# Kernel optimization log

Measured on AMD Instinct MI355X. Metric: run time of the kernel, lower is better.

The kernel has to match this reference:

```python
import jax, jax.numpy as jnp
import numpy as np
from jax import lax

B, C_IN, H, W = 8, 32, 48, 48
C_OUT = 32
K = 3
DEPTH = C_IN * K * K          # 288
L = H * W                      # 2304 (stride=1, pad=1, dil=1 -> same spatial size)


def setup_inputs() -> dict:
    key = jax.random.key(0)
    k1, k2, k3 = jax.random.split(key, 3)
    x = jax.random.normal(k1, (B, C_IN, H, W), dtype=jnp.float32)
    # per-spatial-location unshared weights, same layout as the torch module
    weight = jax.random.normal(k2, (1, DEPTH, L, C_OUT), dtype=jnp.float32) * 0.05
    bias = jax.random.normal(k3, (1, C_OUT, H, W), dtype=jnp.float32) * 0.05
    return {"x": x, "weight": weight, "bias": bias}


def reference(x, weight, bias):
    # unfold: (B, C*K*K, H_out, W_out), channel-major (C, kh, kw) order matches torch unfold
    patches = lax.conv_general_dilated_patches(
        x,
        filter_shape=(K, K),
        window_strides=(1, 1),
        padding=((1, 1), (1, 1)),
        rhs_dilation=(1, 1),
    )
    patches = patches.reshape(B, DEPTH, L)  # (B, depth, L)
    w = weight[0]  # (depth, L, out)
    # fused per-location matmul instead of torch's broadcast-mul + sum
    out = jnp.einsum("bdl,dlo->bol", patches, w)  # (B, out, L)
    return out.reshape(B, C_OUT, H, W) + bias
```

## Files before the change

### kernel.cpp

```cpp
#include <hip/hip_runtime.h>


constexpr int NB    = 8;
constexpr int CIN   = 32;
constexpr int HWD   = 48;
constexpr int COUT  = 32;
constexpr int DEPTH = 288;
constexpr int LTOT  = 2304;
constexpr int LB    = 4;
constexpr int NBLK  = LTOT / LB;
constexpr int PL    = DEPTH * NB + 8;
constexpr int WSTR  = LTOT * COUT;

__global__ __launch_bounds__(256, 3) void lc2d(const float* __restrict__ x,
                                               const float* __restrict__ wgt,
                                               const float* __restrict__ bias,
                                               float* __restrict__ out) {
    __shared__ float patches[LB * PL];
    __shared__ float red[4 * NB * LB * COUT];

    const int tid = threadIdx.x;
    const int bid   = blockIdx.x;
    const int ltile = (bid & 7) * (NBLK / 8) + (bid >> 3);
    const int l0    = ltile * LB;
    const int h0    = l0 / HWD;
    const int w0    = l0 - h0 * HWD;

    #pragma unroll
    for (int k = 0; k < (LB * DEPTH * NB) / 256; ++k) {
        const int sidx = k * 256 + tid;
        const int b  = sidx & 7;
        const int t2 = sidx >> 3;
        const int d  = t2 % DEPTH;
        const int ls = t2 / DEPTH;
        const int c  = d / 9;
        const int r9 = d - c * 9;
        const int kh = r9 / 3;
        const int kw = r9 - kh * 3;
        const int ih = h0 + kh - 1;
        const int iw = w0 + ls + kw - 1;
        float v = 0.f;
        if ((unsigned)ih < (unsigned)HWD && (unsigned)iw < (unsigned)HWD)
            v = x[((b * CIN + c) * HWD + ih) * HWD + iw];
        patches[ls * PL + d * NB + b] = v;
    }
    __syncthreads();

    const int wave = tid >> 6;
    const int lane = tid & 63;
    const int og   = lane & 7;
    const int lsub = (lane >> 3) & 3;
    const int dpar = lane >> 5;
    const int d0   = wave * 72 + dpar * 36;

    const float* wp    = wgt + (size_t)d0 * WSTR + (size_t)(l0 + lsub) * COUT + og * 4;
    const float* pbase = &patches[lsub * PL + d0 * NB];

    float4 acc[NB];
    #pragma unroll
    for (int b = 0; b < NB; ++b) acc[b] = make_float4(0.f, 0.f, 0.f, 0.f);

    float4 wc[4], wn[4];
    #pragma unroll
    for (int j = 0; j < 4; ++j)
        wc[j] = *reinterpret_cast<const float4*>(wp + (size_t)j * WSTR);

    for (int ch = 0; ch < 8; ++ch) {
        #pragma unroll
        for (int j = 0; j < 4; ++j)
            wn[j] = *reinterpret_cast<const float4*>(wp + (size_t)((ch + 1) * 4 + j) * WSTR);
        #pragma unroll
        for (int j = 0; j < 4; ++j) {
            const int i = ch * 4 + j;
            const float4 p0 = *reinterpret_cast<const float4*>(pbase + i * NB);
            const float4 p1 = *reinterpret_cast<const float4*>(pbase + i * NB + 4);
            acc[0].x = fmaf(p0.x, wc[j].x, acc[0].x); acc[0].y = fmaf(p0.x, wc[j].y, acc[0].y);
            acc[0].z = fmaf(p0.x, wc[j].z, acc[0].z); acc[0].w = fmaf(p0.x, wc[j].w, acc[0].w);
            acc[1].x = fmaf(p0.y, wc[j].x, acc[1].x); acc[1].y = fmaf(p0.y, wc[j].y, acc[1].y);
            acc[1].z = fmaf(p0.y, wc[j].z, acc[1].z); acc[1].w = fmaf(p0.y, wc[j].w, acc[1].w);
            acc[2].x = fmaf(p0.z, wc[j].x, acc[2].x); acc[2].y = fmaf(p0.z, wc[j].y, acc[2].y);
            acc[2].z = fmaf(p0.z, wc[j].z, acc[2].z); acc[2].w = fmaf(p0.z, wc[j].w, acc[2].w);
            acc[3].x = fmaf(p0.w, wc[j].x, acc[3].x); acc[3].y = fmaf(p0.w, wc[j].y, acc[3].y);
            acc[3].z = fmaf(p0.w, wc[j].z, acc[3].z); acc[3].w = fmaf(p0.w, wc[j].w, acc[3].w);
            acc[4].x = fmaf(p1.x, wc[j].x, acc[4].x); acc[4].y = fmaf(p1.x, wc[j].y, acc[4].y);
            acc[4].z = fmaf(p1.x, wc[j].z, acc[4].z); acc[4].w = fmaf(p1.x, wc[j].w, acc[4].w);
            acc[5].x = fmaf(p1.y, wc[j].x, acc[5].x); acc[5].y = fmaf(p1.y, wc[j].y, acc[5].y);
            acc[5].z = fmaf(p1.y, wc[j].z, acc[5].z); acc[5].w = fmaf(p1.y, wc[j].w, acc[5].w);
            acc[6].x = fmaf(p1.z, wc[j].x, acc[6].x); acc[6].y = fmaf(p1.z, wc[j].y, acc[6].y);
            acc[6].z = fmaf(p1.z, wc[j].z, acc[6].z); acc[6].w = fmaf(p1.z, wc[j].w, acc[6].w);
            acc[7].x = fmaf(p1.w, wc[j].x, acc[7].x); acc[7].y = fmaf(p1.w, wc[j].y, acc[7].y);
            acc[7].z = fmaf(p1.w, wc[j].z, acc[7].z); acc[7].w = fmaf(p1.w, wc[j].w, acc[7].w);
        }
        #pragma unroll
        for (int j = 0; j < 4; ++j) wc[j] = wn[j];
    }
    #pragma unroll
    for (int j = 0; j < 4; ++j) {
        const int i = 32 + j;
        const float4 p0 = *reinterpret_cast<const float4*>(pbase + i * NB);
        const float4 p1 = *reinterpret_cast<const float4*>(pbase + i * NB + 4);
        acc[0].x = fmaf(p0.x, wc[j].x, acc[0].x); acc[0].y = fmaf(p0.x, wc[j].y, acc[0].y);
        acc[0].z = fmaf(p0.x, wc[j].z, acc[0].z); acc[0].w = fmaf(p0.x, wc[j].w, acc[0].w);
        acc[1].x = fmaf(p0.y, wc[j].x, acc[1].x); acc[1].y = fmaf(p0.y, wc[j].y, acc[1].y);
        acc[1].z = fmaf(p0.y, wc[j].z, acc[1].z); acc[1].w = fmaf(p0.y, wc[j].w, acc[1].w);
        acc[2].x = fmaf(p0.z, wc[j].x, acc[2].x); acc[2].y = fmaf(p0.z, wc[j].y, acc[2].y);
        acc[2].z = fmaf(p0.z, wc[j].z, acc[2].z); acc[2].w = fmaf(p0.z, wc[j].w, acc[2].w);
        acc[3].x = fmaf(p0.w, wc[j].x, acc[3].x); acc[3].y = fmaf(p0.w, wc[j].y, acc[3].y);
        acc[3].z = fmaf(p0.w, wc[j].z, acc[3].z); acc[3].w = fmaf(p0.w, wc[j].w, acc[3].w);
        acc[4].x = fmaf(p1.x, wc[j].x, acc[4].x); acc[4].y = fmaf(p1.x, wc[j].y, acc[4].y);
        acc[4].z = fmaf(p1.x, wc[j].z, acc[4].z); acc[4].w = fmaf(p1.x, wc[j].w, acc[4].w);
        acc[5].x = fmaf(p1.y, wc[j].x, acc[5].x); acc[5].y = fmaf(p1.y, wc[j].y, acc[5].y);
        acc[5].z = fmaf(p1.y, wc[j].z, acc[5].z); acc[5].w = fmaf(p1.y, wc[j].w, acc[5].w);
        acc[6].x = fmaf(p1.z, wc[j].x, acc[6].x); acc[6].y = fmaf(p1.z, wc[j].y, acc[6].y);
        acc[6].z = fmaf(p1.z, wc[j].z, acc[6].z); acc[6].w = fmaf(p1.z, wc[j].w, acc[6].w);
        acc[7].x = fmaf(p1.w, wc[j].x, acc[7].x); acc[7].y = fmaf(p1.w, wc[j].y, acc[7].y);
        acc[7].z = fmaf(p1.w, wc[j].z, acc[7].z); acc[7].w = fmaf(p1.w, wc[j].w, acc[7].w);
    }

    #pragma unroll
    for (int b = 0; b < NB; ++b) {
        acc[b].x += __shfl_xor(acc[b].x, 32);
        acc[b].y += __shfl_xor(acc[b].y, 32);
        acc[b].z += __shfl_xor(acc[b].z, 32);
        acc[b].w += __shfl_xor(acc[b].w, 32);
    }
    if (lane < 32) {
        #pragma unroll
        for (int b = 0; b < NB; ++b)
            *reinterpret_cast<float4*>(&red[(((wave * NB) + b) * LB + lsub) * COUT + og * 4]) = acc[b];
    }
    __syncthreads();

    const int ob = tid >> 5;
    const int oo = tid & 31;
    float s[LB];
    #pragma unroll
    for (int l = 0; l < LB; ++l)
        s[l] = red[((0 * NB + ob) * LB + l) * COUT + oo]
             + red[((1 * NB + ob) * LB + l) * COUT + oo]
             + red[((2 * NB + ob) * LB + l) * COUT + oo]
             + red[((3 * NB + ob) * LB + l) * COUT + oo];
    const float4 bv = *reinterpret_cast<const float4*>(bias + (size_t)oo * LTOT + l0);
    const float4 o4 = make_float4(s[0] + bv.x, s[1] + bv.y, s[2] + bv.z, s[3] + bv.w);
    *reinterpret_cast<float4*>(out + ((size_t)(ob * COUT + oo)) * LTOT + l0) = o4;
}

extern "C" void kernel_launch(void* const* d_in, const int* in_sizes, int n_in,
                              void* d_out, int out_size, void* d_ws, size_t ws_size,
                              hipStream_t stream) {
    const float* x    = (const float*)d_in[0];
    const float* wgt  = (const float*)d_in[1];
    const float* bias = (const float*)d_in[2];
    float* out        = (float*)d_out;
    lc2d<<<NBLK, 256, 0, stream>>>(x, wgt, bias, out);
}
```

Baseline: 29.90 us.

## Alias reduction buffer onto patch LDS and deepen weight prefetch to three stages

The reduction scratch now reuses the patches shared-memory buffer, with an extra barrier before it is overwritten. This cuts LDS per block so four blocks fit per CU instead of three, and the launch bounds are raised to match. The weight loads move from double-buffered to triple-buffered register prefetch, keeping more global loads in flight. The deeper prefetch and higher occupancy target both push on register pressure, which could lead to spills.

```diff
diff --git a/kernel.cpp b/kernel.cpp
--- a/kernel.cpp
+++ b/kernel.cpp
@@ -12,12 +12,42 @@
 constexpr int PL    = DEPTH * NB + 8;
 constexpr int WSTR  = LTOT * COUT;
 
-__global__ __launch_bounds__(256, 3) void lc2d(const float* __restrict__ x,
+#define FMAS(P0, P1, WV)                                                        \
+    acc[0].x = fmaf((P0).x, (WV).x, acc[0].x); acc[0].y = fmaf((P0).x, (WV).y, acc[0].y); \
+    acc[0].z = fmaf((P0).x, (WV).z, acc[0].z); acc[0].w = fmaf((P0).x, (WV).w, acc[0].w); \
+    acc[1].x = fmaf((P0).y, (WV).x, acc[1].x); acc[1].y = fmaf((P0).y, (WV).y, acc[1].y); \
+    acc[1].z = fmaf((P0).y, (WV).z, acc[1].z); acc[1].w = fmaf((P0).y, (WV).w, acc[1].w); \
+    acc[2].x = fmaf((P0).z, (WV).x, acc[2].x); acc[2].y = fmaf((P0).z, (WV).y, acc[2].y); \
+    acc[2].z = fmaf((P0).z, (WV).z, acc[2].z); acc[2].w = fmaf((P0).z, (WV).w, acc[2].w); \
+    acc[3].x = fmaf((P0).w, (WV).x, acc[3].x); acc[3].y = fmaf((P0).w, (WV).y, acc[3].y); \
+    acc[3].z = fmaf((P0).w, (WV).z, acc[3].z); acc[3].w = fmaf((P0).w, (WV).w, acc[3].w); \
+    acc[4].x = fmaf((P1).x, (WV).x, acc[4].x); acc[4].y = fmaf((P1).x, (WV).y, acc[4].y); \
+    acc[4].z = fmaf((P1).x, (WV).z, acc[4].z); acc[4].w = fmaf((P1).x, (WV).w, acc[4].w); \
+    acc[5].x = fmaf((P1).y, (WV).x, acc[5].x); acc[5].y = fmaf((P1).y, (WV).y, acc[5].y); \
+    acc[5].z = fmaf((P1).y, (WV).z, acc[5].z); acc[5].w = fmaf((P1).y, (WV).w, acc[5].w); \
+    acc[6].x = fmaf((P1).z, (WV).x, acc[6].x); acc[6].y = fmaf((P1).z, (WV).y, acc[6].y); \
+    acc[6].z = fmaf((P1).z, (WV).z, acc[6].z); acc[6].w = fmaf((P1).z, (WV).w, acc[6].w); \
+    acc[7].x = fmaf((P1).w, (WV).x, acc[7].x); acc[7].y = fmaf((P1).w, (WV).y, acc[7].y); \
+    acc[7].z = fmaf((P1).w, (WV).z, acc[7].z); acc[7].w = fmaf((P1).w, (WV).w, acc[7].w);
+
+#define PRELOAD(W, CH)                                                          \
+    { _Pragma("unroll") for (int j = 0; j < 4; ++j)                             \
+        W[j] = *reinterpret_cast<const float4*>(wp + (size_t)((CH) * 4 + j) * WSTR); }
+
+#define COMPUTE(W, CH)                                                          \
+    { _Pragma("unroll") for (int j = 0; j < 4; ++j) {                           \
+        const int i = (CH) * 4 + j;                                             \
+        const float4 p0 = *reinterpret_cast<const float4*>(pbase + i * NB);     \
+        const float4 p1 = *reinterpret_cast<const float4*>(pbase + i * NB + 4); \
+        FMAS(p0, p1, W[j]); } }
+
+__global__ __launch_bounds__(256, 4) void lc2d(const float* __restrict__ x,
                                                const float* __restrict__ wgt,
                                                const float* __restrict__ bias,
                                                float* __restrict__ out) {
-    __shared__ float patches[LB * PL];
-    __shared__ float red[4 * NB * LB * COUT];
+    __shared__ float lds[LB * PL];
+    float* const patches = lds;
+    float* const red     = lds;
 
     const int tid = threadIdx.x;
     const int bid   = blockIdx.x;
@@ -60,62 +90,15 @@
     #pragma unroll
     for (int b = 0; b < NB; ++b) acc[b] = make_float4(0.f, 0.f, 0.f, 0.f);
 
-    float4 wc[4], wn[4];
+    float4 wA[4], wB[4], wC[4];
+    PRELOAD(wA, 0) PRELOAD(wB, 1) PRELOAD(wC, 2)
     #pragma unroll
-    for (int j = 0; j < 4; ++j)
-        wc[j] = *reinterpret_cast<const float4*>(wp + (size_t)j * WSTR);
-
-    for (int ch = 0; ch < 8; ++ch) {
-        #pragma unroll
-        for (int j = 0; j < 4; ++j)
-            wn[j] = *reinterpret_cast<const float4*>(wp + (size_t)((ch + 1) * 4 + j) * WSTR);
-        #pragma unroll
-        for (int j = 0; j < 4; ++j) {
-            const int i = ch * 4 + j;
-            const float4 p0 = *reinterpret_cast<const float4*>(pbase + i * NB);
-            const float4 p1 = *reinterpret_cast<const float4*>(pbase + i * NB + 4);
-            acc[0].x = fmaf(p0.x, wc[j].x, acc[0].x); acc[0].y = fmaf(p0.x, wc[j].y, acc[0].y);
-            acc[0].z = fmaf(p0.x, wc[j].z, acc[0].z); acc[0].w = fmaf(p0.x, wc[j].w, acc[0].w);
-            acc[1].x = fmaf(p0.y, wc[j].x, acc[1].x); acc[1].y = fmaf(p0.y, wc[j].y, acc[1].y);
-            acc[1].z = fmaf(p0.y, wc[j].z, acc[1].z); acc[1].w = fmaf(p0.y, wc[j].w, acc[1].w);
-            acc[2].x = fmaf(p0.z, wc[j].x, acc[2].x); acc[2].y = fmaf(p0.z, wc[j].y, acc[2].y);
-            acc[2].z = fmaf(p0.z, wc[j].z, acc[2].z); acc[2].w = fmaf(p0.z, wc[j].w, acc[2].w);
-            acc[3].x = fmaf(p0.w, wc[j].x, acc[3].x); acc[3].y = fmaf(p0.w, wc[j].y, acc[3].y);
-            acc[3].z = fmaf(p0.w, wc[j].z, acc[3].z); acc[3].w = fmaf(p0.w, wc[j].w, acc[3].w);
-            acc[4].x = fmaf(p1.x, wc[j].x, acc[4].x); acc[4].y = fmaf(p1.x, wc[j].y, acc[4].y);
-            acc[4].z = fmaf(p1.x, wc[j].z, acc[4].z); acc[4].w = fmaf(p1.x, wc[j].w, acc[4].w);
-            acc[5].x = fmaf(p1.y, wc[j].x, acc[5].x); acc[5].y = fmaf(p1.y, wc[j].y, acc[5].y);
-            acc[5].z = fmaf(p1.y, wc[j].z, acc[5].z); acc[5].w = fmaf(p1.y, wc[j].w, acc[5].w);
-            acc[6].x = fmaf(p1.z, wc[j].x, acc[6].x); acc[6].y = fmaf(p1.z, wc[j].y, acc[6].y);
-            acc[6].z = fmaf(p1.z, wc[j].z, acc[6].z); acc[6].w = fmaf(p1.z, wc[j].w, acc[6].w);
-            acc[7].x = fmaf(p1.w, wc[j].x, acc[7].x); acc[7].y = fmaf(p1.w, wc[j].y, acc[7].y);
-            acc[7].z = fmaf(p1.w, wc[j].z, acc[7].z); acc[7].w = fmaf(p1.w, wc[j].w, acc[7].w);
-        }
-        #pragma unroll
-        for (int j = 0; j < 4; ++j) wc[j] = wn[j];
+    for (int ch = 0; ch < 6; ch += 3) {
+        COMPUTE(wA, ch)     PRELOAD(wA, ch + 3)
+        COMPUTE(wB, ch + 1) PRELOAD(wB, ch + 4)
+        COMPUTE(wC, ch + 2) PRELOAD(wC, ch + 5)
     }
-    #pragma unroll
-    for (int j = 0; j < 4; ++j) {
-        const int i = 32 + j;
-        const float4 p0 = *reinterpret_cast<const float4*>(pbase + i * NB);
-        const float4 p1 = *reinterpret_cast<const float4*>(pbase + i * NB + 4);
-        acc[0].x = fmaf(p0.x, wc[j].x, acc[0].x); acc[0].y = fmaf(p0.x, wc[j].y, acc[0].y);
-        acc[0].z = fmaf(p0.x, wc[j].z, acc[0].z); acc[0].w = fmaf(p0.x, wc[j].w, acc[0].w);
-        acc[1].x = fmaf(p0.y, wc[j].x, acc[1].x); acc[1].y = fmaf(p0.y, wc[j].y, acc[1].y);
-        acc[1].z = fmaf(p0.y, wc[j].z, acc[1].z); acc[1].w = fmaf(p0.y, wc[j].w, acc[1].w);
-        acc[2].x = fmaf(p0.z, wc[j].x, acc[2].x); acc[2].y = fmaf(p0.z, wc[j].y, acc[2].y);
-        acc[2].z = fmaf(p0.z, wc[j].z, acc[2].z); acc[2].w = fmaf(p0.z, wc[j].w, acc[2].w);
-        acc[3].x = fmaf(p0.w, wc[j].x, acc[3].x); acc[3].y = fmaf(p0.w, wc[j].y, acc[3].y);
-        acc[3].z = fmaf(p0.w, wc[j].z, acc[3].z); acc[3].w = fmaf(p0.w, wc[j].w, acc[3].w);
-        acc[4].x = fmaf(p1.x, wc[j].x, acc[4].x); acc[4].y = fmaf(p1.x, wc[j].y, acc[4].y);
-        acc[4].z = fmaf(p1.x, wc[j].z, acc[4].z); acc[4].w = fmaf(p1.x, wc[j].w, acc[4].w);
-        acc[5].x = fmaf(p1.y, wc[j].x, acc[5].x); acc[5].y = fmaf(p1.y, wc[j].y, acc[5].y);
-        acc[5].z = fmaf(p1.y, wc[j].z, acc[5].z); acc[5].w = fmaf(p1.y, wc[j].w, acc[5].w);
-        acc[6].x = fmaf(p1.z, wc[j].x, acc[6].x); acc[6].y = fmaf(p1.z, wc[j].y, acc[6].y);
-        acc[6].z = fmaf(p1.z, wc[j].z, acc[6].z); acc[6].w = fmaf(p1.z, wc[j].w, acc[6].w);
-        acc[7].x = fmaf(p1.w, wc[j].x, acc[7].x); acc[7].y = fmaf(p1.w, wc[j].y, acc[7].y);
-        acc[7].z = fmaf(p1.w, wc[j].z, acc[7].z); acc[7].w = fmaf(p1.w, wc[j].w, acc[7].w);
-    }
+    COMPUTE(wA, 6) COMPUTE(wB, 7) COMPUTE(wC, 8)
 
     #pragma unroll
     for (int b = 0; b < NB; ++b) {
@@ -124,6 +107,7 @@
         acc[b].z += __shfl_xor(acc[b].z, 32);
         acc[b].w += __shfl_xor(acc[b].w, 32);
     }
+    __syncthreads();
     if (lane < 32) {
         #pragma unroll
         for (int b = 0; b < NB; ++b)
```

Measured after the change: 30.66 us. +2.6%, slower.
